# Kernel tuning notes

Hardware: AMD Instinct MI355X
Metric: run time of the kernel (lower is better)

Reference implementation:

```python
import jax, jax.numpy as jnp
import numpy as np

B, T, C = 8, 2048, 512
KEY_SIZE, VALUE_SIZE = 512, 512


def setup_inputs() -> dict:
    key = jax.random.key(0)
    ks = jax.random.split(key, 7)
    s = 0.02
    return {
        "input": jax.random.normal(ks[0], (B, T, C), dtype=jnp.float32),
        "Wq": jax.random.normal(ks[1], (KEY_SIZE, C), dtype=jnp.float32) * s,
        "bq": jax.random.normal(ks[2], (KEY_SIZE,), dtype=jnp.float32) * s,
        "Wk": jax.random.normal(ks[3], (KEY_SIZE, C), dtype=jnp.float32) * s,
        "bk": jax.random.normal(ks[4], (KEY_SIZE,), dtype=jnp.float32) * s,
        "Wv": jax.random.normal(ks[5], (VALUE_SIZE, C), dtype=jnp.float32) * s,
        "bv": jax.random.normal(ks[6], (VALUE_SIZE,), dtype=jnp.float32) * s,
    }


def reference(input, Wq, bq, Wk, bk, Wv, bv):
    # input: [B, T, C]
    sqrt_key_size = jnp.sqrt(jnp.float32(Wq.shape[0]))
    query = jnp.einsum('btc,kc->btk', input, Wq) + bq   # [B, T, K]
    keys = jnp.einsum('btc,kc->btk', input, Wk) + bk    # [B, T, K]
    values = jnp.einsum('btc,vc->btv', input, Wv) + bv  # [B, T, V]
    # logits[b, j, i] = q_j . k_i
    logits = jnp.einsum('bjk,bik->bji', query, keys)    # [B, T, T]
    # mask[j, i] = True where i > j (future key positions) -> -inf
    j = jnp.arange(logits.shape[1])[:, None]
    i = jnp.arange(logits.shape[2])[None, :]
    mask = i > j
    masked = jnp.where(mask[None, :, :], -jnp.inf, logits)
    # NOTE: original softmaxes over dim=1 (the query axis), non-standard.
    probs = jax.nn.softmax(masked / sqrt_key_size, axis=1)  # [B, T, T]
    read = jnp.einsum('bji,biv->bjv', probs, values)        # [B, T, V]
    return jnp.concatenate((input, read), axis=2)           # [B, T, C+V]
```

## Files before the change

kernel.cpp:

```cpp
#include <hip/hip_runtime.h>

typedef unsigned short u16;
using bf16x8 = __attribute__((ext_vector_type(8))) short;
using f32x4  = __attribute__((ext_vector_type(4))) float;

static __device__ __forceinline__ u16 f2b(float f) {
  unsigned int x = __builtin_bit_cast(unsigned int, f);
  unsigned int r = (x + 0x7fffu + ((x >> 16) & 1u)) >> 16;
  return (u16)r;
}
static __device__ __forceinline__ float fin(float x) { return (x != x) ? 0.f : x; }
static __device__ __forceinline__ float expclamp(float x) {
  return __expf(fminf(fmaxf(x, -80.f), 80.f));
}
static __device__ __forceinline__ unsigned cvt2(float lo, float hi) {
  unsigned r;
  asm("v_cvt_pk_bf16_f32 %0, %1, %2" : "=v"(r) : "v"(lo), "v"(hi));
  return r;
}

#define SCALE 0.04419417382415922f
#define MFMA16(a, b, c) __builtin_amdgcn_mfma_f32_16x16x32_bf16((a), (b), (c), 0, 0, 0)

static __device__ __forceinline__ void glds16(const u16* g, u16* l) {
  __builtin_amdgcn_global_load_lds(
      (const __attribute__((address_space(1))) unsigned int*)(unsigned long long)(const void*)g,
      (__attribute__((address_space(3))) unsigned int*)(unsigned int)(unsigned long long)(void*)l,
      16, 0, 0);
}


__global__ __launch_bounds__(256) void qkv_mfma(
    const float* __restrict__ X,
    const float* __restrict__ Wq, const float* __restrict__ bq,
    const float* __restrict__ Wk, const float* __restrict__ bk,
    const float* __restrict__ Wv, const float* __restrict__ bv,
    u16* __restrict__ outq, u16* __restrict__ Kw, u16* __restrict__ Vt) {
  __shared__ __align__(16) u16 SM[16384];
  u16* As = SM;
  u16* Bs = SM + 8192;
  const int id = blockIdx.x;
  const int xcd = id & 7;
  const int slot = id >> 3;
  const int bxl = slot / 12;
  const int byz = slot - bxl * 12;
  const int z = byz >> 2;
  const int by = byz & 3;
  const int bx = (xcd << 4) + bxl;
  const float* W = (z == 0) ? Wq : ((z == 1) ? Wk : Wv);
  const float* bias = (z == 0) ? bq : ((z == 1) ? bk : bv);
  const int row0 = bx * 128;
  const int col0 = by * 128;
  const int tid = threadIdx.x, lane = tid & 63, w = tid >> 6;
  const int lrow = lane & 15, lg = lane >> 4;
  const int qm = w >> 1, qn = w & 1;
  const int srow = tid >> 1, sh = tid & 1;

  const f32x4 Z4 = {0.f, 0.f, 0.f, 0.f};
  f32x4 acc[4][4];
#pragma unroll
  for (int m = 0; m < 4; ++m)
#pragma unroll
    for (int n = 0; n < 4; ++n) acc[m][n] = Z4;

  const float* Xr = X + (size_t)(row0 + srow) * 512;
  const float* Wr = W + (size_t)(col0 + srow) * 512;

  for (int ks = 0; ks < 8; ++ks) {
    const int k0 = ks * 64;
    __syncthreads();
#pragma unroll
    for (int s4 = 0; s4 < 4; ++s4) {
      const int slt = sh * 4 + s4;
      const int ds = ((slt ^ (srow & 7)) << 3);
      {
        float4 f0 = *(const float4*)(Xr + k0 + slt * 8);
        float4 f1 = *(const float4*)(Xr + k0 + slt * 8 + 4);
        uint4 pk;
        pk.x = cvt2(f0.x, f0.y); pk.y = cvt2(f0.z, f0.w);
        pk.z = cvt2(f1.x, f1.y); pk.w = cvt2(f1.z, f1.w);
        *(uint4*)&As[srow * 64 + ds] = pk;
      }
      {
        float4 f0 = *(const float4*)(Wr + k0 + slt * 8);
        float4 f1 = *(const float4*)(Wr + k0 + slt * 8 + 4);
        uint4 pk;
        pk.x = cvt2(f0.x, f0.y); pk.y = cvt2(f0.z, f0.w);
        pk.z = cvt2(f1.x, f1.y); pk.w = cvt2(f1.z, f1.w);
        *(uint4*)&Bs[srow * 64 + ds] = pk;
      }
    }
    __syncthreads();
#pragma unroll
    for (int cs = 0; cs < 2; ++cs) {
      bf16x8 af[4], bfr[4];
#pragma unroll
      for (int mf = 0; mf < 4; ++mf) {
        const int r = qm * 64 + mf * 16 + lrow;
        af[mf] = *(const bf16x8*)&As[r * 64 + (((cs * 4 + lg) ^ (r & 7)) << 3)];
      }
#pragma unroll
      for (int nf = 0; nf < 4; ++nf) {
        const int r = qn * 64 + nf * 16 + lrow;
        bfr[nf] = *(const bf16x8*)&Bs[r * 64 + (((cs * 4 + lg) ^ (r & 7)) << 3)];
      }
#pragma unroll
      for (int mf = 0; mf < 4; ++mf)
#pragma unroll
        for (int nf = 0; nf < 4; ++nf)
          acc[mf][nf] = MFMA16(af[mf], bfr[nf], acc[mf][nf]);
    }
  }

  if (z < 2) {
    u16* O = (z == 0) ? outq : Kw;
    const int ldo = (z == 0) ? 2048 : 512;
#pragma unroll
    for (int mf = 0; mf < 4; ++mf)
#pragma unroll
      for (int nf = 0; nf < 4; ++nf) {
        const int C = col0 + qn * 64 + nf * 16 + lrow;
        const float bb = bias[C];
#pragma unroll
        for (int r = 0; r < 4; ++r) {
          const int R = row0 + qm * 64 + mf * 16 + lg * 4 + r;
          O[(size_t)R * ldo + C] = f2b(fin(acc[mf][nf][r] + bb));
        }
      }
  } else {
    __syncthreads();
    u16* Tr = SM;
#pragma unroll
    for (int mf = 0; mf < 4; ++mf)
#pragma unroll
      for (int nf = 0; nf < 4; ++nf) {
        const int vl = qn * 64 + nf * 16 + lrow;
        const float bb = bias[col0 + vl];
#pragma unroll
        for (int r = 0; r < 4; ++r) {
          const int tl = qm * 64 + mf * 16 + lg * 4 + r;
          Tr[vl * 128 + tl] = f2b(fin(acc[mf][nf][r] + bb));
        }
      }
    __syncthreads();
    const int vl = tid >> 1, part = tid & 1;
    const int bI = row0 >> 11;
    u16* dst = Vt + (size_t)(bI * 512 + col0 + vl) * 2048 + (row0 & 2047) + part * 64;
    const u16* sp = &Tr[vl * 128 + part * 64];
#pragma unroll
    for (int q = 0; q < 8; ++q)
      *(uint4*)(dst + q * 8) = *(const uint4*)(sp + q * 8);
  }
}

__global__ __launch_bounds__(512, 2) void denom_mfma(
    const u16* __restrict__ Qs, const u16* __restrict__ Kw, float* __restrict__ rdn) {
  __shared__ __align__(16) u16 QB[2][32768];
  __shared__ float red[2][4][16];
  const int id = blockIdx.x;
  const int b = id & 7, px = id >> 3;
  const int tid = threadIdx.x, lane = tid & 63, w = tid >> 6;
  const int lrow = lane & 15, lg = lane >> 4;
  const int ih = w >> 2, jq = w & 3;
  const size_t kbase = (size_t)b * 2048 * 512;
  const f32x4 Z4 = {0.f, 0.f, 0.f, 0.f};

  for (int half = 0; half < 2; ++half) {
    const int it = half ? (63 - px) : px;
    const int i0 = it * 32;
    bf16x8 Kf[16];
    const u16* kr = Kw + kbase + (size_t)(i0 + ih * 16 + lrow) * 512;
#pragma unroll
    for (int cs = 0; cs < 16; ++cs) Kf[cs] = *(const bf16x8*)(kr + cs * 32 + lg * 8);
    float dacc[4] = {0.f, 0.f, 0.f, 0.f};
    const int jstart = i0 & ~63;
    const int NW = (2048 - jstart) >> 6;
#pragma unroll
    for (int p = 0; p < 8; ++p) {
      const int row = p * 8 + w;
      glds16(Qs + (size_t)(b * 2048 + jstart + row) * 2048 + ((lane ^ (row & 7)) << 3),
             &QB[0][row * 512]);
    }
    for (int win = 0; win < NW; ++win) {
      const int cur = win & 1;
      const int j0w = jstart + win * 64;
      if (win + 1 < NW) {
#pragma unroll
        for (int p = 0; p < 8; ++p) {
          const int row = p * 8 + w;
          glds16(Qs + (size_t)(b * 2048 + j0w + 64 + row) * 2048 + ((lane ^ (row & 7)) << 3),
                 &QB[cur ^ 1][row * 512]);
        }
        asm volatile("s_waitcnt vmcnt(8)" ::: "memory");
      } else {
        asm volatile("s_waitcnt vmcnt(0)" ::: "memory");
      }
      __builtin_amdgcn_s_barrier();
      const u16* qb = &QB[cur][0];
      const int qrow = jq * 16 + lrow;
      f32x4 sA = Z4, sB = Z4;
#pragma unroll
      for (int cs = 0; cs < 8; ++cs) {
        bf16x8 q0 = *(const bf16x8*)(qb + qrow * 512 + (((cs * 4 + lg) ^ (qrow & 7)) << 3));
        bf16x8 q1 = *(const bf16x8*)(qb + qrow * 512 + ((((cs + 8) * 4 + lg) ^ (qrow & 7)) << 3));
        sA = MFMA16(Kf[cs], q0, sA);
        sB = MFMA16(Kf[cs + 8], q1, sB);
      }
      const int jG = j0w + jq * 16 + lrow;
      const int ib = i0 + ih * 16 + lg * 4;
#pragma unroll
      for (int r = 0; r < 4; ++r) {
        float e = (jG >= ib + r) ? expclamp((sA[r] + sB[r]) * SCALE) : 0.f;
        e += __shfl_xor(e, 1); e += __shfl_xor(e, 2);
        e += __shfl_xor(e, 4); e += __shfl_xor(e, 8);
        dacc[r] += e;
      }
      asm volatile("s_waitcnt lgkmcnt(0)" ::: "memory");
      __builtin_amdgcn_s_barrier();
    }
    if (lrow == 0) {
#pragma unroll
      for (int r = 0; r < 4; ++r) red[ih][jq][lg * 4 + r] = dacc[r];
    }
    __syncthreads();
    if (tid < 32) {
      const int ihh = tid >> 4, il = tid & 15;
      const float d = red[ihh][0][il] + red[ihh][1][il] + red[ihh][2][il] + red[ihh][3][il];
      rdn[(size_t)(b * 2048 + i0 + ihh * 16 + il) * 1024 + 256] = d;
    }
    __syncthreads();
  }
}

__global__ __launch_bounds__(512, 2) void read_mfma(
    const u16* __restrict__ Qs, const u16* __restrict__ Kw, const u16* __restrict__ Vt,
    const float* __restrict__ rdn, float* __restrict__ outf) {
  __shared__ __align__(16) u16 KB[2][32768];
  __shared__ __align__(16) u16 PB[32 * 72];
  const int id = blockIdx.x;
  const int b = id & 7, px = id >> 3;
  const int tid = threadIdx.x, lane = tid & 63, w = tid >> 6;
  const int lrow = lane & 15, lg = lane >> 4;
  const int jh = w >> 2, q4 = w & 3;
  const size_t kbase = (size_t)b * 2048 * 512;
  const size_t vbase = (size_t)b * 512 * 2048;
  const f32x4 Z4 = {0.f, 0.f, 0.f, 0.f};

  for (int half = 0; half < 2; ++half) {
    const int jt = half ? (63 - px) : px;
    const int j0 = jt * 32;
    const int NW = (jt + 2) >> 1;

    bf16x8 Qf[16];
    const u16* qr = Qs + (size_t)(b * 2048 + j0 + jh * 16 + lrow) * 2048;
#pragma unroll
    for (int cs = 0; cs < 16; ++cs) Qf[cs] = *(const bf16x8*)(qr + cs * 32 + lg * 8);
    f32x4 O[8];
#pragma unroll
    for (int t = 0; t < 8; ++t) O[t] = Z4;

#pragma unroll
    for (int p = 0; p < 8; ++p) {
      const int row = p * 8 + w;
      glds16(Kw + kbase + (size_t)row * 512 + ((lane ^ (row & 7)) << 3),
             &KB[0][row * 512]);
    }

    for (int win = 0; win < NW; ++win) {
      const int cur = win & 1;
      const int i0 = win * 64;
      bf16x8 Vp[16];
#pragma unroll
      for (int t = 0; t < 8; ++t)
#pragma unroll
        for (int is = 0; is < 2; ++is)
          Vp[t * 2 + is] = *(const bf16x8*)(
              Vt + vbase + (size_t)(q4 * 128 + t * 16 + lrow) * 2048 + i0 + is * 32 + lg * 8);
      const float dsum = rdn[(size_t)(b * 2048 + i0 + q4 * 16 + lrow) * 1024 + 256];
      if (win + 1 < NW) {
        const int ni = i0 + 64;
#pragma unroll
        for (int p = 0; p < 8; ++p) {
          const int row = p * 8 + w;
          glds16(Kw + kbase + (size_t)(ni + row) * 512 + ((lane ^ (row & 7)) << 3),
                 &KB[cur ^ 1][row * 512]);
        }
        asm volatile("s_waitcnt vmcnt(25)" ::: "memory");
      } else {
        asm volatile("s_waitcnt vmcnt(17)" ::: "memory");
      }
      __builtin_amdgcn_s_barrier();

      const u16* kb = &KB[cur][0];
      const int krow = q4 * 16 + lrow;
      f32x4 sA = Z4, sB = Z4;
#pragma unroll
      for (int cs = 0; cs < 8; ++cs) {
        bf16x8 k0 = *(const bf16x8*)(kb + krow * 512 + (((cs * 4 + lg) ^ (krow & 7)) << 3));
        bf16x8 k1 = *(const bf16x8*)(kb + krow * 512 + ((((cs + 8) * 4 + lg) ^ (krow & 7)) << 3));
        sA = MFMA16(Qf[cs], k0, sA);
        sB = MFMA16(Qf[cs + 8], k1, sB);
      }
      if (win + 1 < NW) asm volatile("s_waitcnt vmcnt(8)" ::: "memory");
      else              asm volatile("s_waitcnt vmcnt(0)" ::: "memory");
      const float rd = 1.0f / fmaxf(dsum, 1e-30f);
      const int iG = i0 + q4 * 16 + lrow;
      const int jb = j0 + jh * 16 + lg * 4;
#pragma unroll
      for (int r = 0; r < 4; ++r) {
        const float e = (iG <= jb + r) ? expclamp((sA[r] + sB[r]) * SCALE) * rd : 0.f;
        PB[(jh * 16 + lg * 4 + r) * 72 + q4 * 16 + lrow] = f2b(e);
      }
      asm volatile("s_waitcnt lgkmcnt(0)" ::: "memory");
      __builtin_amdgcn_s_barrier();

      const bf16x8 pa0 = *(const bf16x8*)&PB[(jh * 16 + lrow) * 72 + lg * 8];
      const bf16x8 pa1 = *(const bf16x8*)&PB[(jh * 16 + lrow) * 72 + 32 + lg * 8];
#pragma unroll
      for (int t = 0; t < 8; ++t) {
        O[t] = MFMA16(pa0, Vp[t * 2 + 0], O[t]);
        O[t] = MFMA16(pa1, Vp[t * 2 + 1], O[t]);
      }
    }

#pragma unroll
    for (int t = 0; t < 8; ++t) {
      const int v = q4 * 128 + t * 16 + lrow;
#pragma unroll
      for (int r = 0; r < 4; ++r) {
        const int jj = j0 + jh * 16 + lg * 4 + r;
        outf[(size_t)(b * 2048 + jj) * 1024 + 512 + v] = fin(O[t][r]);
      }
    }
    __syncthreads();
  }
}

__global__ __launch_bounds__(256) void copy_in_kernel(
    const float* __restrict__ X, float* __restrict__ outf) {
  size_t idx = (size_t)blockIdx.x * 256 + threadIdx.x;
  size_t row = idx >> 7;
  int c = (int)(idx & 127) * 4;
  *(float4*)&outf[row * 1024 + c] = *(const float4*)&X[row * 512 + c];
}

extern "C" void kernel_launch(void* const* d_in, const int* in_sizes, int n_in,
                              void* d_out, int out_size, void* d_ws, size_t ws_size,
                              hipStream_t stream) {
  const float* X  = (const float*)d_in[0];
  const float* Wq = (const float*)d_in[1];
  const float* bq = (const float*)d_in[2];
  const float* Wk = (const float*)d_in[3];
  const float* bk = (const float*)d_in[4];
  const float* Wv = (const float*)d_in[5];
  const float* bv = (const float*)d_in[6];

  char* ws = (char*)d_ws;
  const size_t SZ = (size_t)16384 * 512 * sizeof(u16);
  u16* Kw = (u16*)(ws);
  u16* Vt = (u16*)(ws + SZ);

  qkv_mfma<<<dim3(1536), 256, 0, stream>>>(X, Wq, bq, Wk, bk, Wv, bv,
                                           (u16*)d_out, Kw, Vt);
  denom_mfma<<<dim3(256), 512, 0, stream>>>((const u16*)d_out, Kw, (float*)d_out);
  read_mfma<<<dim3(256), 512, 0, stream>>>((const u16*)d_out, Kw, Vt,
                                           (const float*)d_out, (float*)d_out);
  copy_in_kernel<<<8192, 256, 0, stream>>>(X, (float*)d_out);
}
```

Measured before the change: 452.8 us.

## Split denom over j-stripes and warp-specialize read kernel into score/PV roles

The denominator kernel now splits each key tile's query range into four interleaved stripes across more blocks. It uses smaller 32-row LDS tiles and writes four partial sums, which the read kernel adds together. The read kernel drops the two-tile loop per block and runs one 32-row query tile per block. It is warp-specialized: four warps compute masked exp scores into a double-buffered P tile, while the other four accumulate P·V one step behind. This is meant to overlap the QK and PV phases and raise occupancy, at the cost of more blocks, half the warps idle in each phase, and an extra pipeline step.

```diff
diff --git a/kernel.cpp b/kernel.cpp
--- a/kernel.cpp
+++ b/kernel.cpp
@@ -153,61 +153,62 @@
   }
 }
 
-__global__ __launch_bounds__(512, 2) void denom_mfma(
+__global__ __launch_bounds__(512, 4) void denom_mfma(
     const u16* __restrict__ Qs, const u16* __restrict__ Kw, float* __restrict__ rdn) {
-  __shared__ __align__(16) u16 QB[2][32768];
-  __shared__ float red[2][4][16];
+  __shared__ __align__(16) u16 QB[2][16384];
+  __shared__ float red[4][2][16];
   const int id = blockIdx.x;
-  const int b = id & 7, px = id >> 3;
+  const int b = id & 7, rest = id >> 3;
+  const int py = rest >> 2, stripe = rest & 3;
   const int tid = threadIdx.x, lane = tid & 63, w = tid >> 6;
   const int lrow = lane & 15, lg = lane >> 4;
-  const int ih = w >> 2, jq = w & 3;
+  const int ihh = w >> 1, jq = w & 1;
   const size_t kbase = (size_t)b * 2048 * 512;
   const f32x4 Z4 = {0.f, 0.f, 0.f, 0.f};
 
-  for (int half = 0; half < 2; ++half) {
-    const int it = half ? (63 - px) : px;
-    const int i0 = it * 32;
+  for (int pass = 0; pass < 2; ++pass) {
+    const int ti = pass ? (31 - py) : py;
+    const int i0 = ti * 64;
     bf16x8 Kf[16];
-    const u16* kr = Kw + kbase + (size_t)(i0 + ih * 16 + lrow) * 512;
+    const u16* kr = Kw + kbase + (size_t)(i0 + ihh * 16 + lrow) * 512;
 #pragma unroll
     for (int cs = 0; cs < 16; ++cs) Kf[cs] = *(const bf16x8*)(kr + cs * 32 + lg * 8);
     float dacc[4] = {0.f, 0.f, 0.f, 0.f};
-    const int jstart = i0 & ~63;
-    const int NW = (2048 - jstart) >> 6;
-#pragma unroll
-    for (int p = 0; p < 8; ++p) {
-      const int row = p * 8 + w;
-      glds16(Qs + (size_t)(b * 2048 + jstart + row) * 2048 + ((lane ^ (row & 7)) << 3),
-             &QB[0][row * 512]);
-    }
-    for (int win = 0; win < NW; ++win) {
-      const int cur = win & 1;
-      const int j0w = jstart + win * 64;
-      if (win + 1 < NW) {
-#pragma unroll
-        for (int p = 0; p < 8; ++p) {
+    const int m0 = (i0 >> 5) + stripe;
+
+    if (m0 <= 63) {
+#pragma unroll
+      for (int p = 0; p < 4; ++p) {
+        const int row = p * 8 + w;
+        glds16(Qs + (size_t)(b * 2048 + m0 * 32 + row) * 2048 + ((lane ^ (row & 7)) << 3),
+               &QB[0][row * 512]);
+      }
+    }
+    __syncthreads();
+
+    int n = 0;
+    for (int m = m0; m <= 63; m += 4, ++n) {
+      const int cur = n & 1;
+      if (m + 4 <= 63) {
+#pragma unroll
+        for (int p = 0; p < 4; ++p) {
           const int row = p * 8 + w;
-          glds16(Qs + (size_t)(b * 2048 + j0w + 64 + row) * 2048 + ((lane ^ (row & 7)) << 3),
+          glds16(Qs + (size_t)(b * 2048 + (m + 4) * 32 + row) * 2048 + ((lane ^ (row & 7)) << 3),
                  &QB[cur ^ 1][row * 512]);
         }
-        asm volatile("s_waitcnt vmcnt(8)" ::: "memory");
-      } else {
-        asm volatile("s_waitcnt vmcnt(0)" ::: "memory");
-      }
-      __builtin_amdgcn_s_barrier();
+      }
       const u16* qb = &QB[cur][0];
       const int qrow = jq * 16 + lrow;
       f32x4 sA = Z4, sB = Z4;
 #pragma unroll
       for (int cs = 0; cs < 8; ++cs) {
-        bf16x8 q0 = *(const bf16x8*)(qb + qrow * 512 + (((cs * 4 + lg) ^ (qrow & 7)) << 3));
-        bf16x8 q1 = *(const bf16x8*)(qb + qrow * 512 + ((((cs + 8) * 4 + lg) ^ (qrow & 7)) << 3));
+        bf16x8 q0 = *(const bf16x8*)(qb + qrow * 512 + (((cs * 4 + lg) ^ (lrow & 7)) << 3));
+        bf16x8 q1 = *(const bf16x8*)(qb + qrow * 512 + (((32 + cs * 4 + lg) ^ (lrow & 7)) << 3));
         sA = MFMA16(Kf[cs], q0, sA);
         sB = MFMA16(Kf[cs + 8], q1, sB);
       }
-      const int jG = j0w + jq * 16 + lrow;
-      const int ib = i0 + ih * 16 + lg * 4;
+      const int jG = m * 32 + jq * 16 + lrow;
+      const int ib = i0 + ihh * 16 + lg * 4;
 #pragma unroll
       for (int r = 0; r < 4; ++r) {
         float e = (jG >= ib + r) ? expclamp((sA[r] + sB[r]) * SCALE) : 0.f;
@@ -215,124 +216,126 @@
         e += __shfl_xor(e, 4); e += __shfl_xor(e, 8);
         dacc[r] += e;
       }
-      asm volatile("s_waitcnt lgkmcnt(0)" ::: "memory");
-      __builtin_amdgcn_s_barrier();
-    }
+      __syncthreads();
+    }
+
     if (lrow == 0) {
 #pragma unroll
-      for (int r = 0; r < 4; ++r) red[ih][jq][lg * 4 + r] = dacc[r];
-    }
-    __syncthreads();
-    if (tid < 32) {
-      const int ihh = tid >> 4, il = tid & 15;
-      const float d = red[ihh][0][il] + red[ihh][1][il] + red[ihh][2][il] + red[ihh][3][il];
-      rdn[(size_t)(b * 2048 + i0 + ihh * 16 + il) * 1024 + 256] = d;
-    }
-    __syncthreads();
-  }
-}
-
-__global__ __launch_bounds__(512, 2) void read_mfma(
+      for (int r = 0; r < 4; ++r) red[ihh][jq][lg * 4 + r] = dacc[r];
+    }
+    __syncthreads();
+    if (tid < 64) {
+      const float d = red[tid >> 4][0][tid & 15] + red[tid >> 4][1][tid & 15];
+      rdn[(size_t)(b * 2048 + i0 + tid) * 1024 + 256 + stripe] = d;
+    }
+    __syncthreads();
+  }
+}
+
+__global__ __launch_bounds__(512, 4) void read_mfma(
     const u16* __restrict__ Qs, const u16* __restrict__ Kw, const u16* __restrict__ Vt,
     const float* __restrict__ rdn, float* __restrict__ outf) {
-  __shared__ __align__(16) u16 KB[2][32768];
-  __shared__ __align__(16) u16 PB[32 * 72];
+  __shared__ __align__(16) u16 KB[2][16384];
+  __shared__ __align__(16) u16 PB[2][32 * 40];
   const int id = blockIdx.x;
-  const int b = id & 7, px = id >> 3;
+  const int b = id & 7, s = id >> 3;
+  const int jt = (s < 32) ? s : 95 - s;
+  const int j0 = jt * 32;
   const int tid = threadIdx.x, lane = tid & 63, w = tid >> 6;
   const int lrow = lane & 15, lg = lane >> 4;
-  const int jh = w >> 2, q4 = w & 3;
+  const int role = w >> 2, wq = w & 3;
+  const int jh = wq >> 1, iq = wq & 1;
+  const int vq = wq;
+  const int NW = jt + 1;
   const size_t kbase = (size_t)b * 2048 * 512;
   const size_t vbase = (size_t)b * 512 * 2048;
   const f32x4 Z4 = {0.f, 0.f, 0.f, 0.f};
 
-  for (int half = 0; half < 2; ++half) {
-    const int jt = half ? (63 - px) : px;
-    const int j0 = jt * 32;
-    const int NW = (jt + 2) >> 1;
-
-    bf16x8 Qf[16];
+  f32x4 RS[16];
+  if (role == 0) {
     const u16* qr = Qs + (size_t)(b * 2048 + j0 + jh * 16 + lrow) * 2048;
 #pragma unroll
-    for (int cs = 0; cs < 16; ++cs) Qf[cs] = *(const bf16x8*)(qr + cs * 32 + lg * 8);
-    f32x4 O[8];
-#pragma unroll
-    for (int t = 0; t < 8; ++t) O[t] = Z4;
-
-#pragma unroll
-    for (int p = 0; p < 8; ++p) {
-      const int row = p * 8 + w;
-      glds16(Kw + kbase + (size_t)row * 512 + ((lane ^ (row & 7)) << 3),
-             &KB[0][row * 512]);
-    }
-
-    for (int win = 0; win < NW; ++win) {
-      const int cur = win & 1;
-      const int i0 = win * 64;
-      bf16x8 Vp[16];
-#pragma unroll
-      for (int t = 0; t < 8; ++t)
-#pragma unroll
-        for (int is = 0; is < 2; ++is)
-          Vp[t * 2 + is] = *(const bf16x8*)(
-              Vt + vbase + (size_t)(q4 * 128 + t * 16 + lrow) * 2048 + i0 + is * 32 + lg * 8);
-      const float dsum = rdn[(size_t)(b * 2048 + i0 + q4 * 16 + lrow) * 1024 + 256];
-      if (win + 1 < NW) {
-        const int ni = i0 + 64;
-#pragma unroll
-        for (int p = 0; p < 8; ++p) {
-          const int row = p * 8 + w;
-          glds16(Kw + kbase + (size_t)(ni + row) * 512 + ((lane ^ (row & 7)) << 3),
-                 &KB[cur ^ 1][row * 512]);
-        }
-        asm volatile("s_waitcnt vmcnt(25)" ::: "memory");
-      } else {
-        asm volatile("s_waitcnt vmcnt(17)" ::: "memory");
-      }
-      __builtin_amdgcn_s_barrier();
-
-      const u16* kb = &KB[cur][0];
-      const int krow = q4 * 16 + lrow;
-      f32x4 sA = Z4, sB = Z4;
-#pragma unroll
-      for (int cs = 0; cs < 8; ++cs) {
-        bf16x8 k0 = *(const bf16x8*)(kb + krow * 512 + (((cs * 4 + lg) ^ (krow & 7)) << 3));
-        bf16x8 k1 = *(const bf16x8*)(kb + krow * 512 + ((((cs + 8) * 4 + lg) ^ (krow & 7)) << 3));
-        sA = MFMA16(Qf[cs], k0, sA);
-        sB = MFMA16(Qf[cs + 8], k1, sB);
-      }
-      if (win + 1 < NW) asm volatile("s_waitcnt vmcnt(8)" ::: "memory");
-      else              asm volatile("s_waitcnt vmcnt(0)" ::: "memory");
-      const float rd = 1.0f / fmaxf(dsum, 1e-30f);
-      const int iG = i0 + q4 * 16 + lrow;
-      const int jb = j0 + jh * 16 + lg * 4;
-#pragma unroll
-      for (int r = 0; r < 4; ++r) {
-        const float e = (iG <= jb + r) ? expclamp((sA[r] + sB[r]) * SCALE) * rd : 0.f;
-        PB[(jh * 16 + lg * 4 + r) * 72 + q4 * 16 + lrow] = f2b(e);
-      }
-      asm volatile("s_waitcnt lgkmcnt(0)" ::: "memory");
-      __builtin_amdgcn_s_barrier();
-
-      const bf16x8 pa0 = *(const bf16x8*)&PB[(jh * 16 + lrow) * 72 + lg * 8];
-      const bf16x8 pa1 = *(const bf16x8*)&PB[(jh * 16 + lrow) * 72 + 32 + lg * 8];
-#pragma unroll
-      for (int t = 0; t < 8; ++t) {
-        O[t] = MFMA16(pa0, Vp[t * 2 + 0], O[t]);
-        O[t] = MFMA16(pa1, Vp[t * 2 + 1], O[t]);
-      }
-    }
-
-#pragma unroll
-    for (int t = 0; t < 8; ++t) {
-      const int v = q4 * 128 + t * 16 + lrow;
-#pragma unroll
-      for (int r = 0; r < 4; ++r) {
-        const int jj = j0 + jh * 16 + lg * 4 + r;
-        outf[(size_t)(b * 2048 + jj) * 1024 + 512 + v] = fin(O[t][r]);
-      }
-    }
-    __syncthreads();
+    for (int cs = 0; cs < 16; ++cs)
+      RS[cs] = __builtin_bit_cast(f32x4, *(const bf16x8*)(qr + cs * 32 + lg * 8));
+  } else {
+#pragma unroll
+    for (int t = 0; t < 16; ++t) RS[t] = Z4;
+  }
+
+#pragma unroll
+  for (int p = 0; p < 4; ++p) {
+    const int row = p * 8 + w;
+    glds16(Kw + kbase + (size_t)row * 512 + ((lane ^ (row & 7)) << 3),
+           &KB[0][row * 512]);
+  }
+  __syncthreads();
+
+  for (int t = 0; t <= NW; ++t) {
+    if (t + 1 < NW) {
+#pragma unroll
+      for (int p = 0; p < 4; ++p) {
+        const int row = p * 8 + w;
+        glds16(Kw + kbase + (size_t)((t + 1) * 32 + row) * 512 + ((lane ^ (row & 7)) << 3),
+               &KB[(t + 1) & 1][row * 512]);
+      }
+    }
+    if (role == 0) {
+      if (t < NW) {
+        const int i0 = t * 32;
+        const int iG = i0 + iq * 16 + lrow;
+        const float4 rp = *(const float4*)&rdn[(size_t)(b * 2048 + iG) * 1024 + 256];
+        const u16* kb = &KB[t & 1][0];
+        const int krow = iq * 16 + lrow;
+        f32x4 sA = Z4, sB = Z4;
+#pragma unroll
+        for (int cs = 0; cs < 8; ++cs) {
+          bf16x8 k0 = *(const bf16x8*)(kb + krow * 512 + (((cs * 4 + lg) ^ (lrow & 7)) << 3));
+          bf16x8 k1 = *(const bf16x8*)(kb + krow * 512 + (((32 + cs * 4 + lg) ^ (lrow & 7)) << 3));
+          sA = MFMA16(__builtin_bit_cast(bf16x8, RS[cs]), k0, sA);
+          sB = MFMA16(__builtin_bit_cast(bf16x8, RS[cs + 8]), k1, sB);
+        }
+        const float rd = 1.0f / fmaxf(rp.x + rp.y + rp.z + rp.w, 1e-30f);
+        const int jb = j0 + jh * 16 + lg * 4;
+#pragma unroll
+        for (int r = 0; r < 4; ++r) {
+          const float e = (iG <= jb + r) ? expclamp((sA[r] + sB[r]) * SCALE) * rd : 0.f;
+          PB[t & 1][(jh * 16 + lg * 4 + r) * 40 + iq * 16 + lrow] = f2b(e);
+        }
+      }
+    } else {
+      if (t >= 1) {
+        const int i0 = (t - 1) * 32;
+        bf16x8 Vp[8];
+#pragma unroll
+        for (int vt = 0; vt < 8; ++vt)
+          Vp[vt] = *(const bf16x8*)(
+              Vt + vbase + (size_t)(vq * 128 + vt * 16 + lrow) * 2048 + i0 + lg * 8);
+        const u16* pb = &PB[(t - 1) & 1][0];
+        const bf16x8 pa0 = *(const bf16x8*)(pb + lrow * 40 + lg * 8);
+        const bf16x8 pa1 = *(const bf16x8*)(pb + (16 + lrow) * 40 + lg * 8);
+#pragma unroll
+        for (int vt = 0; vt < 8; ++vt) {
+          RS[vt] = MFMA16(pa0, Vp[vt], RS[vt]);
+          RS[8 + vt] = MFMA16(pa1, Vp[vt], RS[8 + vt]);
+        }
+      }
+    }
+    __syncthreads();
+  }
+
+  if (role == 1) {
+#pragma unroll
+    for (int jh2 = 0; jh2 < 2; ++jh2)
+#pragma unroll
+      for (int vt = 0; vt < 8; ++vt) {
+        const int v = vq * 128 + vt * 16 + lrow;
+        const f32x4 o = RS[jh2 * 8 + vt];
+#pragma unroll
+        for (int r = 0; r < 4; ++r) {
+          const int jj = j0 + jh2 * 16 + lg * 4 + r;
+          outf[(size_t)(b * 2048 + jj) * 1024 + 512 + v] = fin(o[r]);
+        }
+      }
   }
 }
 
@@ -362,8 +365,8 @@
 
   qkv_mfma<<<dim3(1536), 256, 0, stream>>>(X, Wq, bq, Wk, bk, Wv, bv,
                                            (u16*)d_out, Kw, Vt);
-  denom_mfma<<<dim3(256), 512, 0, stream>>>((const u16*)d_out, Kw, (float*)d_out);
-  read_mfma<<<dim3(256), 512, 0, stream>>>((const u16*)d_out, Kw, Vt,
+  denom_mfma<<<dim3(512), 512, 0, stream>>>((const u16*)d_out, Kw, (float*)d_out);
+  read_mfma<<<dim3(512), 512, 0, stream>>>((const u16*)d_out, Kw, Vt,
                                            (const float*)d_out, (float*)d_out);
   copy_in_kernel<<<8192, 256, 0, stream>>>(X, (float*)d_out);
 }
```

New measurement: 381.4 us. 15.8% less time.
